# Optimization experiments

Measured on AMD Instinct MI355X. Metric: run time of the kernel, lower is better.

The kernel has to match this reference:

```python
import jax, jax.numpy as jnp
import numpy as np

L, H = 3, 8
B, N, D, E = 4, 256, 128, 128
NH, EH1, EH2 = 512, 512, 512


def _ln(x, g, b):
    m = x.mean(-1, keepdims=True)
    v = ((x - m) ** 2).mean(-1, keepdims=True)
    return (x - m) * jax.lax.rsqrt(v + 1e-5) * g + b


def setup_inputs() -> dict:
    key = jax.random.key(0)
    ks = jax.random.split(key, 16)
    w = lambda k, *s: jax.random.normal(k, s, jnp.float32) * 0.02
    inp = {
        'node_features': jax.random.normal(ks[0], (B, N, D), jnp.float32),
        'edge_features': jax.random.normal(ks[1], (B, N, N, E), jnp.float32),
        'Wqkv_n': w(ks[2], L, D, 3 * D), 'bqkv_n': jnp.zeros((L, 3 * D)),
        'Wqkv_e': w(ks[3], L, E, 3 * D), 'bqkv_e': jnp.zeros((L, 3 * D)),
        'Wo': w(ks[4], L, D, D), 'bo': jnp.zeros((L, D)),
        'Wn1': w(ks[5], L, D, NH), 'bn1': jnp.zeros((L, NH)),
        'Wn2': w(ks[6], L, NH, D), 'bn2': jnp.zeros((L, D)),
        'ln1n_g': jnp.ones((L, D)), 'ln1n_b': jnp.zeros((L, D)),
        'ln2n_g': jnp.ones((L, D)), 'ln2n_b': jnp.zeros((L, D)),
        'We1a': w(ks[7], L, 2 * D + 2 * E, EH1), 'be1a': jnp.zeros((L, EH1)),
        'We1b': w(ks[8], L, EH1, E), 'be1b': jnp.zeros((L, E)),
        'We2a': w(ks[9], L, E, EH2), 'be2a': jnp.zeros((L, EH2)),
        'We2b': w(ks[10], L, EH2, E), 'be2b': jnp.zeros((L, E)),
        'ln1e_g': jnp.ones((L, E)), 'ln1e_b': jnp.zeros((L, E)),
        'ln2e_g': jnp.ones((L, E)), 'ln2e_b': jnp.zeros((L, E)),
    }
    return inp


def reference(node_features, edge_features, Wqkv_n, bqkv_n, Wqkv_e, bqkv_e, Wo, bo,
              Wn1, bn1, Wn2, bn2, ln1n_g, ln1n_b, ln2n_g, ln2n_b,
              We1a, be1a, We1b, be1b, We2a, be2a, We2b, be2b,
              ln1e_g, ln1e_b, ln2e_g, ln2e_b):
    n, e = node_features, edge_features
    b_, N_, D_ = n.shape
    hd = D_ // H
    scale = 1.0 / np.sqrt(hd).astype(np.float32)
    for l in range(Wqkv_n.shape[0]):
        # ---- edge-biased attention ----
        qkv_n = (n @ Wqkv_n[l] + bqkv_n[l]).reshape(b_, N_, H, 3 * hd).transpose(0, 2, 1, 3)  # B,H,N,3hd
        q_n, k_n, v_n = jnp.split(qkv_n, 3, axis=-1)
        qkv_e = (e @ Wqkv_e[l] + bqkv_e[l]).reshape(b_, N_, N_, H, 3 * hd).transpose(0, 3, 1, 2, 4)  # B,H,N,N,3hd
        q_e, k_e, v_e = jnp.split(qkv_e, 3, axis=-1)
        q = q_n[:, :, :, None, :] + q_e  # B,H,N,N,hd
        # NOTE: the original torch code overwrites k with q (`k = q.reshape(...)`),
        # so scores are the squared norm of q; k_n/k_e are dead code. Faithful.
        scores = jnp.einsum('bhijd,bhijd->bhij', q, q) * scale
        att = jax.nn.softmax(scores, axis=-1)
        v = v_n[:, :, None, :, :] + v_e  # B,H,N,N,hd
        out = jnp.einsum('bhij,bhijd->bhid', att, v)  # B,H,N,hd
        out = out.transpose(0, 2, 1, 3).reshape(b_, N_, D_) @ Wo[l] + bo[l]
        n = _ln(n + out, ln1n_g[l], ln1n_b[l])
        ff = jax.nn.relu(n @ Wn1[l] + bn1[l]) @ Wn2[l] + bn2[l]
        n = _ln(n + ff, ln2n_g[l], ln2n_b[l])
        # ---- edge update ----
        src = jnp.broadcast_to(n[:, None, :, :], (b_, N_, N_, D_))  # node j
        tgt = jnp.broadcast_to(n[:, :, None, :], (b_, N_, N_, D_))  # node i
        cat = jnp.concatenate([e, e.transpose(0, 2, 1, 3), src, tgt], axis=-1)
        e1 = jax.nn.relu(cat @ We1a[l] + be1a[l]) @ We1b[l] + be1b[l]
        e = _ln(e + e1, ln1e_g[l], ln1e_b[l])
        e2 = jax.nn.relu(e @ We2a[l] + be2a[l]) @ We2b[l] + be2b[l]
        e = _ln(e + e2, ln2e_g[l], ln2e_b[l])
    return n
```

## Files before the change

kernel.cpp:

```cpp
#include <hip/hip_runtime.h>

typedef unsigned short u16;
typedef __bf16 bf16x8 __attribute__((ext_vector_type(8)));
typedef float f32x4 __attribute__((ext_vector_type(4)));

#define NB 4
#define NN 256
#define DD 128
#define RNN 262144

__device__ __forceinline__ u16 f2b(float f) {
    unsigned u = __builtin_bit_cast(unsigned, f);
    unsigned rb = ((u >> 16) & 1u) + 0x7FFFu;
    return (u16)((u + rb) >> 16);
}
__device__ __forceinline__ float b2f(u16 u) {
    return __builtin_bit_cast(float, ((unsigned)u) << 16);
}
__device__ __forceinline__ u16 b16(float f) {
    __bf16 h = (__bf16)f;
    return __builtin_bit_cast(u16, h);
}
__device__ __forceinline__ unsigned pk2(float a, float b) {
    ushort2 r;
    r.x = b16(a); r.y = b16(b);
    return __builtin_bit_cast(unsigned, r);
}

__device__ __forceinline__ void glds16(const void* g, void* l) {
    __builtin_amdgcn_global_load_lds((const __attribute__((address_space(1))) void*)g,
                                     (__attribute__((address_space(3))) void*)l, 16, 0, 0);
}

__global__ void prep_weights(const float* __restrict__ Wqkv_e, const float* __restrict__ bqkv_e,
                             const float* __restrict__ We1a, const float* __restrict__ We1b,
                             const float* __restrict__ We2a, const float* __restrict__ We2b,
                             u16* wqT, u16* wv, float* bqp, float* bvp,
                             u16* w1f_e1, u16* w2f_e1, u16* w1f_e2, u16* w2f_e2) {
    int l = blockIdx.z, sec = blockIdx.y;
    int idx = blockIdx.x * 256 + threadIdx.x;
    if (sec == 0) {
        if (idx < 16384) {
            int n = idx >> 7, k = idx & 127;
            int col = (n >> 4) * 48 + (n & 15);
            wqT[l * 16384 + n * 128 + k] = f2b(Wqkv_e[l * 49152 + k * 384 + col]);
        }
    } else if (sec == 1) {
        if (idx < 16384) {
            int k = idx >> 7, c = idx & 127;
            int col = (c >> 4) * 48 + 32 + (c & 15);
            wv[l * 16384 + k * 128 + c] = f2b(Wqkv_e[l * 49152 + k * 384 + col]);
        }
        if (idx < 128) {
            bqp[l * 128 + idx] = bqkv_e[l * 384 + (idx >> 4) * 48 + (idx & 15)];
            bvp[l * 128 + idx] = bqkv_e[l * 384 + (idx >> 4) * 48 + 32 + (idx & 15)];
        }
    } else if (sec == 2) {
        if (idx < 131072) {
            int step = idx >> 13, q = step >> 2, kt = step & 3;
            int rem = idx & 8191;
            int nb = rem >> 10, ks = (rem >> 9) & 1, ln = (rem >> 3) & 63, j = rem & 7;
            int n = q * 128 + nb * 16 + (ln & 15);
            int k = kt * 64 + ks * 32 + (ln >> 4) * 8 + j;
            w1f_e1[l * 131072 + idx] = f2b(We1a[l * 262144 + k * 512 + n]);
        }
    } else if (sec == 3) {
        if (idx < 65536) {
            int step = idx >> 13, q = step >> 1, kt2 = step & 1;
            int rem = idx & 8191;
            int cb = rem >> 10, ks = (rem >> 9) & 1, ln = (rem >> 3) & 63, j = rem & 7;
            int c = cb * 16 + (ln & 15);
            int k = q * 128 + kt2 * 64 + ks * 32 + (ln >> 4) * 8 + j;
            w2f_e1[l * 65536 + idx] = f2b(We1b[l * 65536 + k * 128 + c]);
        }
    } else if (sec == 4) {
        if (idx < 65536) {
            int step = idx >> 13, q = step >> 1, kt = step & 1;
            int rem = idx & 8191;
            int nb = rem >> 10, ks = (rem >> 9) & 1, ln = (rem >> 3) & 63, j = rem & 7;
            int n = q * 128 + nb * 16 + (ln & 15);
            int k = kt * 64 + ks * 32 + (ln >> 4) * 8 + j;
            w1f_e2[l * 65536 + idx] = f2b(We2a[l * 65536 + k * 512 + n]);
        }
    } else {
        if (idx < 65536) {
            int step = idx >> 13, q = step >> 1, kt2 = step & 1;
            int rem = idx & 8191;
            int cb = rem >> 10, ks = (rem >> 9) & 1, ln = (rem >> 3) & 63, j = rem & 7;
            int c = cb * 16 + (ln & 15);
            int k = q * 128 + kt2 * 64 + ks * 32 + (ln >> 4) * 8 + j;
            w2f_e2[l * 65536 + idx] = f2b(We2b[l * 65536 + k * 128 + c]);
        }
    }
}

__global__ void init_e(const float4* __restrict__ src, ushort4* __restrict__ dst) {
    const long n4 = 8388608;
    for (long i = (long)blockIdx.x * blockDim.x + threadIdx.x; i < n4; i += (long)gridDim.x * blockDim.x) {
        float4 v = src[i];
        ushort4 o;
        o.x = f2b(v.x); o.y = f2b(v.y); o.z = f2b(v.z); o.w = f2b(v.w);
        dst[i] = o;
    }
}

__global__ void init_n(const float* __restrict__ node, float* __restrict__ nf) {
    int i = blockIdx.x * 256 + threadIdx.x;
    if (i < 131072) nf[i] = node[i];
}

__launch_bounds__(512)
__global__ void pre_node_kernel(const float* __restrict__ nf, const float* __restrict__ We1a,
                                float* __restrict__ preS, float* __restrict__ preT) {
    __shared__ float nr[128];
    int tid = threadIdx.x;
    int row = blockIdx.x;
    if (tid < 128) nr[tid] = nf[(long)row * 128 + tid];
    __syncthreads();
    int c = tid;
    float s = 0.f, t = 0.f;
    const float* Ws = We1a + (long)256 * 512 + c;
    const float* Wt = We1a + (long)384 * 512 + c;
    #pragma unroll 8
    for (int k = 0; k < 128; ++k) {
        float nv = nr[k];
        s += nv * Ws[k * 512];
        t += nv * Wt[k * 512];
    }
    preS[(long)row * 512 + c] = s;
    preT[(long)row * 512 + c] = t;
}

__global__ void qkvn_kernel(const float* __restrict__ nf, const float* __restrict__ W,
                            const float* __restrict__ bias, float* __restrict__ qn, float* __restrict__ vn) {
    __shared__ float nr[128];
    int tid = threadIdx.x;
    int row = blockIdx.x;
    if (tid < 128) nr[tid] = nf[(long)row * 128 + tid];
    __syncthreads();
    int c = tid & 127;
    bool isq = tid < 128;
    int col = (c >> 4) * 48 + (c & 15) + (isq ? 0 : 32);
    float a = bias[col];
    #pragma unroll 8
    for (int k = 0; k < 128; ++k) a += nr[k] * W[k * 384 + col];
    if (isq) qn[(long)row * 128 + c] = a;
    else     vn[(long)row * 128 + c] = a;
}

__launch_bounds__(256, 2)
__global__ void scores_kernel(const u16* __restrict__ ein, const u16* __restrict__ WqT,
                              const float* __restrict__ bqp, const float* __restrict__ qn,
                              float* __restrict__ scoresp) {
    __shared__ u16 As[128 * 64];
    __shared__ u16 Bs[128 * 64];
    int tid = threadIdx.x;
    int wid = tid >> 6, lane = tid & 63;
    int bid = blockIdx.x;
    int jhalf = bid & 1, bi = bid >> 1;
    int b = bi >> 8, i = bi & 255;
    int wr = wid >> 1, wc = wid & 1;

    f32x4 acc[4][4];
    f32x4 z = {0.f, 0.f, 0.f, 0.f};
    #pragma unroll
    for (int m = 0; m < 4; ++m)
        #pragma unroll
        for (int n = 0; n < 4; ++n) acc[m][n] = z;

    const long arow0 = ((long)(b * NN + i) * NN + jhalf * 128);
    for (int kt = 0; kt < 2; ++kt) {
        int k0 = kt << 6;
        #pragma unroll
        for (int p = 0; p < 4; ++p) {
            int r = p * 32 + (tid >> 3);
            int ch = tid & 7;
            const u16* src = ein + (arow0 + r) * 128 + k0 + ((ch ^ (r & 7)) << 3);
            glds16(src, (char*)As + (p << 12) + (wid << 10));
            int n = p * 32 + (tid >> 3);
            const u16* bsrc = WqT + (long)n * 128 + k0 + ((ch ^ (n & 7)) << 3);
            glds16(bsrc, (char*)Bs + (p << 12) + (wid << 10));
        }
        __syncthreads();
        #pragma unroll
        for (int ks = 0; ks < 2; ++ks) {
            bf16x8 af[4], bfr[4];
            #pragma unroll
            for (int m = 0; m < 4; ++m) {
                int r = wr * 64 + m * 16 + (lane & 15);
                int ch = (ks * 4 + (lane >> 4)) ^ (r & 7);
                af[m] = *reinterpret_cast<const bf16x8*>(&As[r * 64 + ch * 8]);
            }
            #pragma unroll
            for (int n = 0; n < 4; ++n) {
                int c = wc * 64 + n * 16 + (lane & 15);
                int ch = (ks * 4 + (lane >> 4)) ^ (c & 7);
                bfr[n] = *reinterpret_cast<const bf16x8*>(&Bs[c * 64 + ch * 8]);
            }
            #pragma unroll
            for (int m = 0; m < 4; ++m)
                #pragma unroll
                for (int n = 0; n < 4; ++n)
                    acc[m][n] = __builtin_amdgcn_mfma_f32_16x16x32_bf16(af[m], bfr[n], acc[m][n], 0, 0, 0);
        }
        __syncthreads();
    }
    const float* qnb = qn + (long)(b * NN + i) * 128;
    #pragma unroll
    for (int m = 0; m < 4; ++m) {
        #pragma unroll
        for (int n = 0; n < 4; ++n) {
            int col = wc * 64 + n * 16 + (lane & 15);
            float add = bqp[col] + qnb[col];
            float sv[4];
            #pragma unroll
            for (int t = 0; t < 4; ++t) { float qv = acc[m][n][t] + add; sv[t] = qv * qv; }
            #pragma unroll
            for (int mk = 1; mk <= 8; mk <<= 1)
                #pragma unroll
                for (int t = 0; t < 4; ++t) sv[t] += __shfl_xor(sv[t], mk);
            if ((lane & 15) == 0) {
                int head = wc * 4 + n;
                int jb = jhalf * 128 + wr * 64 + m * 16 + ((lane >> 4) << 2);
                long sbase = ((long)(b * 8 + head) * 256 + i) * 256 + jb;
                #pragma unroll
                for (int t = 0; t < 4; ++t) scoresp[sbase + t] = sv[t] * 0.25f;
            }
        }
    }
}

__launch_bounds__(256)
__global__ void attn_pv_kernel(const float* __restrict__ scoresp, const u16* __restrict__ ein,
                               const float* __restrict__ vn, const u16* __restrict__ Wv,
                               const float* __restrict__ bvp, float* __restrict__ attn_o) {
    __shared__ float s_s[8 * 256];
    __shared__ float g_s[8 * 128];
    __shared__ float part[256];
    int tid = threadIdx.x;
    int b = blockIdx.x >> 8, i = blockIdx.x & 255;
    for (int v = tid; v < 2048; v += 256) {
        int h = v >> 8, j = v & 255;
        s_s[v] = scoresp[((long)(b * 8 + h) * 256 + i) * 256 + j];
    }
    __syncthreads();
    {
        int h = tid >> 5, lg = tid & 31;
        float vals[8], mx = -1e30f;
        #pragma unroll
        for (int t = 0; t < 8; ++t) { vals[t] = s_s[h * 256 + lg + t * 32]; mx = fmaxf(mx, vals[t]); }
        #pragma unroll
        for (int mk = 16; mk; mk >>= 1) mx = fmaxf(mx, __shfl_xor(mx, mk));
        float sum = 0.f;
        #pragma unroll
        for (int t = 0; t < 8; ++t) { vals[t] = __expf(vals[t] - mx); sum += vals[t]; }
        #pragma unroll
        for (int mk = 16; mk; mk >>= 1) sum += __shfl_xor(sum, mk);
        float inv = 1.f / sum;
        #pragma unroll
        for (int t = 0; t < 8; ++t) s_s[h * 256 + lg + t * 32] = vals[t] * inv;
    }
    __syncthreads();
    {
        int k = tid & 127, h0 = tid >> 7;
        const u16* erow = ein + ((long)(b * NN + i) * NN) * 128 + k;
        float a0 = 0, a1 = 0, a2 = 0, a3 = 0;
        for (int j = 0; j < 256; ++j) {
            float ev = b2f(erow[(long)j * 128]);
            a0 += s_s[(h0    ) * 256 + j] * ev;
            a1 += s_s[(h0 + 2) * 256 + j] * ev;
            a2 += s_s[(h0 + 4) * 256 + j] * ev;
            a3 += s_s[(h0 + 6) * 256 + j] * ev;
        }
        g_s[(h0    ) * 128 + k] = a0;
        g_s[(h0 + 2) * 128 + k] = a1;
        g_s[(h0 + 4) * 128 + k] = a2;
        g_s[(h0 + 6) * 128 + k] = a3;
    }
    __syncthreads();
    {
        int c = tid & 127, half = tid >> 7;
        int h = c >> 4;
        float a = 0.f;
        for (int j = half * 128; j < half * 128 + 128; ++j)
            a += s_s[h * 256 + j] * vn[((long)(b * NN + j)) * 128 + c];
        for (int k = half * 64; k < half * 64 + 64; ++k)
            a += g_s[h * 128 + k] * b2f(Wv[k * 128 + c]);
        part[tid] = a;
    }
    __syncthreads();
    if (tid < 128)
        attn_o[((long)(b * NN + i)) * 128 + tid] = part[tid] + part[128 + tid] + bvp[tid];
}

__launch_bounds__(256)
__global__ void node_kernel(const float* __restrict__ attn_o, float* __restrict__ nf,
                            const float* __restrict__ Wo, const float* __restrict__ bo,
                            const float* __restrict__ Wn1, const float* __restrict__ bn1,
                            const float* __restrict__ Wn2, const float* __restrict__ bn2,
                            const float* __restrict__ g1, const float* __restrict__ b1,
                            const float* __restrict__ g2, const float* __restrict__ b2) {
    __shared__ float ao[128], nr[128], n1[128], hb[512];
    __shared__ float red[8];
    int tid = threadIdx.x;
    int wid = tid >> 6, lane = tid & 63;
    long base = (long)blockIdx.x * 128;
    if (tid < 128) { ao[tid] = attn_o[base + tid]; nr[tid] = nf[base + tid]; }
    __syncthreads();
    float x = 0.f;
    if (tid < 128) {
        float a = bo[tid];
        #pragma unroll 8
        for (int k = 0; k < 128; ++k) a += ao[k] * Wo[k * 128 + tid];
        x = nr[tid] + a;
    }
    float s = (tid < 128) ? x : 0.f, q = (tid < 128) ? x * x : 0.f;
    #pragma unroll
    for (int mk = 1; mk <= 32; mk <<= 1) { s += __shfl_xor(s, mk); q += __shfl_xor(q, mk); }
    if (lane == 0) { red[wid * 2] = s; red[wid * 2 + 1] = q; }
    __syncthreads();
    float sum = red[0] + red[2] + red[4] + red[6];
    float sq  = red[1] + red[3] + red[5] + red[7];
    float mean = sum * (1.f / 128.f);
    float var = sq * (1.f / 128.f) - mean * mean;
    float rs = rsqrtf(var + 1e-5f);
    __syncthreads();
    if (tid < 128) n1[tid] = (x - mean) * rs * g1[tid] + b1[tid];
    __syncthreads();
    for (int c = tid; c < 512; c += 256) {
        float a = bn1[c];
        #pragma unroll 8
        for (int k = 0; k < 128; ++k) a += n1[k] * Wn1[k * 512 + c];
        hb[c] = a > 0.f ? a : 0.f;
    }
    __syncthreads();
    float y = 0.f;
    if (tid < 128) {
        float a = bn2[tid];
        #pragma unroll 8
        for (int k = 0; k < 512; ++k) a += hb[k] * Wn2[k * 128 + tid];
        y = n1[tid] + a;
    }
    float s2 = (tid < 128) ? y : 0.f, q2 = (tid < 128) ? y * y : 0.f;
    #pragma unroll
    for (int mk = 1; mk <= 32; mk <<= 1) { s2 += __shfl_xor(s2, mk); q2 += __shfl_xor(q2, mk); }
    if (lane == 0) { red[wid * 2] = s2; red[wid * 2 + 1] = q2; }
    __syncthreads();
    sum = red[0] + red[2] + red[4] + red[6];
    sq  = red[1] + red[3] + red[5] + red[7];
    mean = sum * (1.f / 128.f);
    var = sq * (1.f / 128.f) - mean * mean;
    rs = rsqrtf(var + 1e-5f);
    if (tid < 128) {
        float o = (y - mean) * rs * g2[tid] + b2[tid];
        nf[base + tid] = o;
    }
}

__launch_bounds__(256, 3)
__global__ void fused_mlp6(const u16* __restrict__ W1aF, const float* __restrict__ b1a,
                           const u16* __restrict__ W1bF, const float* __restrict__ b1b,
                           const u16* __restrict__ W2aF, const float* __restrict__ b2a,
                           const u16* __restrict__ W2bF, const float* __restrict__ b2b,
                           const u16* __restrict__ ein,
                           const float* __restrict__ preS, const float* __restrict__ preT,
                           const float* __restrict__ ln1g, const float* __restrict__ ln1b,
                           const float* __restrict__ ln2g, const float* __restrict__ ln2b,
                           u16* __restrict__ e_dst) {
    __shared__ __align__(16) u16 A_lds[16384];
    __shared__ __align__(16) u16 Hs[8192];
    __shared__ float psum[256], psq[256];

    int tid = threadIdx.x;
    int wid = tid >> 6, lane = tid & 63;
    long row0 = (long)blockIdx.x * 64;
    int b = (int)(row0 >> 16);
    int rem0 = (int)(row0 & 65535);
    int i_ = rem0 >> 8, j0 = rem0 & 255;

    #pragma unroll
    for (int kt = 0; kt < 4; ++kt)
        #pragma unroll
        for (int pp = 0; pp < 2; ++pp) {
            int r = pp * 32 + (tid >> 3);
            int ch = tid & 7;
            long ridx = (kt < 2) ? (long)(b * NN + i_) * NN + (j0 + r)
                                 : (long)(b * NN + (j0 + r)) * NN + i_;
            const u16* src = ein + ridx * DD + ((kt & 1) << 6) + ((ch ^ (r & 7)) << 3);
            glds16(src, (char*)A_lds + kt * 8192 + (pp << 12) + (wid << 10));
        }
    asm volatile("s_waitcnt vmcnt(0)" ::: "memory");
    __builtin_amdgcn_sched_barrier(0);
    __builtin_amdgcn_s_barrier();
    __builtin_amdgcn_sched_barrier(0);

    const u16* w1a = W1aF + (wid * 2) * 1024 + lane * 8;
    const u16* w1b = W1bF + (wid * 2) * 1024 + lane * 8;
    const u16* w2a = W2aF + (wid * 2) * 1024 + lane * 8;
    const u16* w2b = W2bF + (wid * 2) * 1024 + lane * 8;

    f32x4 z = {0.f, 0.f, 0.f, 0.f};
    f32x4 acc1[2][4], acc2[4][2];
    bf16x8 afA[4], afB[4], g2A[4], g2B[4];

    auto FR4 = [&](bf16x8 (&d)[4], const u16* base, int step) {
        const u16* p = base + (step << 13);
        d[0] = *reinterpret_cast<const bf16x8*>(p);
        d[1] = *reinterpret_cast<const bf16x8*>(p + 1024);
        d[2] = *reinterpret_cast<const bf16x8*>(p + 512);
        d[3] = *reinterpret_cast<const bf16x8*>(p + 1536);
    };
    auto G1K = [&](bf16x8 (&cur)[4], int reg) {
        #pragma unroll
        for (int ks = 0; ks < 2; ++ks) {
            bf16x8 bfr[4];
            #pragma unroll
            for (int rf = 0; rf < 4; ++rf) {
                int r = rf * 16 + (lane & 15);
                int ch = (ks * 4 + (lane >> 4)) ^ (r & 7);
                bfr[rf] = *reinterpret_cast<const bf16x8*>(&A_lds[reg * 4096 + r * 64 + ch * 8]);
            }
            #pragma unroll
            for (int mn = 0; mn < 2; ++mn)
                #pragma unroll
                for (int rf = 0; rf < 4; ++rf)
                    acc1[mn][rf] = __builtin_amdgcn_mfma_f32_16x16x32_bf16(cur[ks * 2 + mn], bfr[rf], acc1[mn][rf], 0, 0, 0);
        }
    };
    auto G2K = [&](bf16x8 (&w)[4], int kt2) {
        #pragma unroll
        for (int ks = 0; ks < 2; ++ks) {
            bf16x8 af2[4];
            #pragma unroll
            for (int rf = 0; rf < 4; ++rf) {
                int r = rf * 16 + (lane & 15);
                int c8 = kt2 * 8 + ks * 4 + (lane >> 4);
                int cs = (c8 & 8) | ((c8 ^ r) & 7);
                af2[rf] = *reinterpret_cast<const bf16x8*>((const char*)Hs + r * 256 + cs * 16);
            }
            #pragma unroll
            for (int rf = 0; rf < 4; ++rf)
                #pragma unroll
                for (int cf = 0; cf < 2; ++cf)
                    acc2[rf][cf] = __builtin_amdgcn_mfma_f32_16x16x32_bf16(af2[rf], w[ks * 2 + cf], acc2[rf][cf], 0, 0, 0);
        }
    };
    auto EPI = [&](int q, const float* bias, bool wp) {
        #pragma unroll
        for (int mn = 0; mn < 2; ++mn) {
            int nl0 = wid * 32 + mn * 16 + ((lane >> 4) << 2);
            int n0g = (q << 7) + nl0;
            float4 bb = *reinterpret_cast<const float4*>(&bias[n0g]);
            if (wp) {
                float4 pt = *reinterpret_cast<const float4*>(&preT[(long)(b * NN + i_) * 512 + n0g]);
                bb.x += pt.x; bb.y += pt.y; bb.z += pt.z; bb.w += pt.w;
            }
            #pragma unroll
            for (int rf = 0; rf < 4; ++rf) {
                int r = rf * 16 + (lane & 15);
                float b0 = bb.x, b1_ = bb.y, b2_ = bb.z, b3 = bb.w;
                if (wp) {
                    float4 ps = *reinterpret_cast<const float4*>(&preS[(long)(b * NN + j0 + r) * 512 + n0g]);
                    b0 += ps.x; b1_ += ps.y; b2_ += ps.z; b3 += ps.w;
                }
                float v0 = acc1[mn][rf][0] + b0; v0 = v0 > 0.f ? v0 : 0.f;
                float v1 = acc1[mn][rf][1] + b1_; v1 = v1 > 0.f ? v1 : 0.f;
                float v2 = acc1[mn][rf][2] + b2_; v2 = v2 > 0.f ? v2 : 0.f;
                float v3 = acc1[mn][rf][3] + b3; v3 = v3 > 0.f ? v3 : 0.f;
                uint2 pk;
                pk.x = pk2(v0, v1);
                pk.y = pk2(v2, v3);
                int c8 = nl0 >> 3;
                int cs = (c8 & 8) | ((c8 ^ r) & 7);
                *reinterpret_cast<uint2*>((char*)Hs + r * 256 + cs * 16 + (nl0 & 7) * 2) = pk;
            }
        }
    };
    auto LNA = [&](const float* bias, int rb) {
        #pragma unroll
        for (int rf = 0; rf < 4; ++rf) {
            float sv[4] = {0.f, 0.f, 0.f, 0.f}, qv[4] = {0.f, 0.f, 0.f, 0.f};
            #pragma unroll
            for (int cf = 0; cf < 2; ++cf) {
                int c = wid * 32 + cf * 16 + (lane & 15);
                float bb = bias[c];
                int kk = c & 63, kreg = rb + (c >> 6);
                #pragma unroll
                for (int t = 0; t < 4; ++t) {
                    int r = rf * 16 + ((lane >> 4) << 2) + t;
                    float er = b2f(A_lds[kreg * 4096 + r * 64 + (((kk >> 3) ^ (r & 7)) << 3) + (kk & 7)]);
                    float x = acc2[rf][cf][t] + bb + er;
                    acc2[rf][cf][t] = x;
                    sv[t] += x;
                    qv[t] += x * x;
                }
            }
            #pragma unroll
            for (int mk = 1; mk <= 8; mk <<= 1)
                #pragma unroll
                for (int t = 0; t < 4; ++t) { sv[t] += __shfl_xor(sv[t], mk); qv[t] += __shfl_xor(qv[t], mk); }
            if ((lane & 15) == 0) {
                #pragma unroll
                for (int t = 0; t < 4; ++t) {
                    int r = rf * 16 + ((lane >> 4) << 2) + t;
                    psum[r * 4 + wid] = sv[t];
                    psq[r * 4 + wid] = qv[t];
                }
            }
        }
    };

    #pragma unroll
    for (int rf = 0; rf < 4; ++rf) { acc2[rf][0] = z; acc2[rf][1] = z; }
    FR4(afA, w1a, 0);
    for (int q = 0; q < 4; ++q) {
        #pragma unroll
        for (int mn = 0; mn < 2; ++mn)
            #pragma unroll
            for (int rf = 0; rf < 4; ++rf) acc1[mn][rf] = z;
        FR4(afB, w1a, q * 4 + 1); G1K(afA, 0);
        FR4(afA, w1a, q * 4 + 2); G1K(afB, 1);
        FR4(afB, w1a, q * 4 + 3); G1K(afA, 2);
        G1K(afB, 3);
        FR4(g2A, w1b, q * 2 + 0);
        if (q) {
            __builtin_amdgcn_sched_barrier(0);
            __builtin_amdgcn_s_barrier();
            __builtin_amdgcn_sched_barrier(0);
        }
        EPI(q, b1a, true);
        asm volatile("s_waitcnt lgkmcnt(0)" ::: "memory");
        __builtin_amdgcn_sched_barrier(0);
        __builtin_amdgcn_s_barrier();
        __builtin_amdgcn_sched_barrier(0);
        FR4(g2B, w1b, q * 2 + 1);
        G2K(g2A, 0);
        if (q < 3) FR4(afA, w1a, (q + 1) * 4);
        G2K(g2B, 1);
    }

    LNA(b1b, 0);
    __syncthreads();
    #pragma unroll
    for (int rf = 0; rf < 4; ++rf) {
        #pragma unroll
        for (int t = 0; t < 4; ++t) {
            int r = rf * 16 + ((lane >> 4) << 2) + t;
            float sum = psum[r * 4] + psum[r * 4 + 1] + psum[r * 4 + 2] + psum[r * 4 + 3];
            float sq  = psq[r * 4] + psq[r * 4 + 1] + psq[r * 4 + 2] + psq[r * 4 + 3];
            float mean = sum * (1.f / 128.f);
            float var = sq * (1.f / 128.f) - mean * mean;
            float rs = rsqrtf(var + 1e-5f);
            #pragma unroll
            for (int cf = 0; cf < 2; ++cf) {
                int c = wid * 32 + cf * 16 + (lane & 15);
                float o = (acc2[rf][cf][t] - mean) * rs * ln1g[c] + ln1b[c];
                int kk = c & 63;
                A_lds[(2 + (c >> 6)) * 4096 + r * 64 + (((kk >> 3) ^ (r & 7)) << 3) + (kk & 7)] = b16(o);
            }
        }
    }
    __syncthreads();

    #pragma unroll
    for (int rf = 0; rf < 4; ++rf) { acc2[rf][0] = z; acc2[rf][1] = z; }
    FR4(afA, w2a, 0);
    for (int q = 0; q < 4; ++q) {
        #pragma unroll
        for (int mn = 0; mn < 2; ++mn)
            #pragma unroll
            for (int rf = 0; rf < 4; ++rf) acc1[mn][rf] = z;
        FR4(afB, w2a, q * 2 + 1); G1K(afA, 2);
        G1K(afB, 3);
        FR4(g2A, w2b, q * 2 + 0);
        if (q) {
            __builtin_amdgcn_sched_barrier(0);
            __builtin_amdgcn_s_barrier();
            __builtin_amdgcn_sched_barrier(0);
        }
        EPI(q, b2a, false);
        asm volatile("s_waitcnt lgkmcnt(0)" ::: "memory");
        __builtin_amdgcn_sched_barrier(0);
        __builtin_amdgcn_s_barrier();
        __builtin_amdgcn_sched_barrier(0);
        FR4(g2B, w2b, q * 2 + 1);
        G2K(g2A, 0);
        if (q < 3) FR4(afA, w2a, (q + 1) * 2);
        G2K(g2B, 1);
    }

    LNA(b2b, 2);
    __syncthreads();
    #pragma unroll
    for (int rf = 0; rf < 4; ++rf) {
        #pragma unroll
        for (int t = 0; t < 4; ++t) {
            int r = rf * 16 + ((lane >> 4) << 2) + t;
            float sum = psum[r * 4] + psum[r * 4 + 1] + psum[r * 4 + 2] + psum[r * 4 + 3];
            float sq  = psq[r * 4] + psq[r * 4 + 1] + psq[r * 4 + 2] + psq[r * 4 + 3];
            float mean = sum * (1.f / 128.f);
            float var = sq * (1.f / 128.f) - mean * mean;
            float rs = rsqrtf(var + 1e-5f);
            #pragma unroll
            for (int cf = 0; cf < 2; ++cf) {
                int c = wid * 32 + cf * 16 + (lane & 15);
                float o = (acc2[rf][cf][t] - mean) * rs * ln2g[c] + ln2b[c];
                A_lds[r * 128 + c] = b16(o);
            }
        }
    }
    __syncthreads();
    #pragma unroll
    for (int pp = 0; pp < 4; ++pp) {
        ulonglong2 v = *reinterpret_cast<const ulonglong2*>((char*)A_lds + (pp << 12) + tid * 16);
        *reinterpret_cast<ulonglong2*>((char*)e_dst + row0 * 256 + (pp << 12) + tid * 16) = v;
    }
}

extern "C" void kernel_launch(void* const* d_in, const int* in_sizes, int n_in,
                              void* d_out, int out_size, void* d_ws, size_t ws_size,
                              hipStream_t stream) {
    (void)in_sizes; (void)n_in; (void)out_size; (void)ws_size;
    const float* node   = (const float*)d_in[0];
    const float* edge   = (const float*)d_in[1];
    const float* Wqkv_n = (const float*)d_in[2];
    const float* bqkv_n = (const float*)d_in[3];
    const float* Wqkv_e = (const float*)d_in[4];
    const float* bqkv_e = (const float*)d_in[5];
    const float* Wo     = (const float*)d_in[6];
    const float* bo     = (const float*)d_in[7];
    const float* Wn1    = (const float*)d_in[8];
    const float* bn1    = (const float*)d_in[9];
    const float* Wn2    = (const float*)d_in[10];
    const float* bn2    = (const float*)d_in[11];
    const float* ln1n_g = (const float*)d_in[12];
    const float* ln1n_b = (const float*)d_in[13];
    const float* ln2n_g = (const float*)d_in[14];
    const float* ln2n_b = (const float*)d_in[15];
    const float* We1a   = (const float*)d_in[16];
    const float* be1a   = (const float*)d_in[17];
    const float* We1b   = (const float*)d_in[18];
    const float* be1b   = (const float*)d_in[19];
    const float* We2a   = (const float*)d_in[20];
    const float* be2a   = (const float*)d_in[21];
    const float* We2b   = (const float*)d_in[22];
    const float* be2b   = (const float*)d_in[23];
    const float* ln1e_g = (const float*)d_in[24];
    const float* ln1e_b = (const float*)d_in[25];
    const float* ln2e_g = (const float*)d_in[26];
    const float* ln2e_b = (const float*)d_in[27];

    size_t off = 0;
    char* wsb = (char*)d_ws;
    auto alloc = [&](size_t bytes) -> void* {
        void* p = wsb + off;
        off = (off + bytes + 255) & ~(size_t)255;
        return p;
    };
    u16* eb0      = (u16*)alloc((size_t)RNN * 128 * 2);
    u16* eb1      = (u16*)alloc((size_t)RNN * 128 * 2);
    float* scoresp= (float*)alloc((size_t)2097152 * 4);
    float* qn     = (float*)alloc(131072 * 4);
    float* vn     = (float*)alloc(131072 * 4);
    float* attn_o = (float*)alloc(131072 * 4);
    float* nf     = (float*)alloc(131072 * 4);
    float* preS   = (float*)alloc((size_t)1024 * 512 * 4);
    float* preT   = (float*)alloc((size_t)1024 * 512 * 4);
    u16* wqT      = (u16*)alloc(3 * 16384 * 2);
    u16* wv       = (u16*)alloc(3 * 16384 * 2);
    float* bqp    = (float*)alloc(3 * 128 * 4);
    float* bvp    = (float*)alloc(3 * 128 * 4);
    u16* w1f_e1   = (u16*)alloc(3 * 131072ull * 2);
    u16* w2f_e1   = (u16*)alloc(3 * 65536 * 2);
    u16* w1f_e2   = (u16*)alloc(3 * 65536 * 2);
    u16* w2f_e2   = (u16*)alloc(3 * 65536 * 2);

    {
        dim3 g(512, 6, 3);
        prep_weights<<<g, 256, 0, stream>>>(Wqkv_e, bqkv_e, We1a, We1b, We2a, We2b,
                                            wqT, wv, bqp, bvp, w1f_e1, w2f_e1, w1f_e2, w2f_e2);
    }
    init_e<<<2048, 256, 0, stream>>>((const float4*)edge, (ushort4*)eb0);
    init_n<<<512, 256, 0, stream>>>(node, nf);

    for (int l = 0; l < 3; ++l) {
        u16* ein  = (l & 1) ? eb1 : eb0;
        u16* eout = (l & 1) ? eb0 : eb1;
        qkvn_kernel<<<1024, 256, 0, stream>>>(nf, Wqkv_n + l * 49152, bqkv_n + l * 384, qn, vn);
        scores_kernel<<<2048, 256, 0, stream>>>(ein, wqT + l * 16384, bqp + l * 128, qn, scoresp);
        attn_pv_kernel<<<1024, 256, 0, stream>>>(scoresp, ein, vn, wv + l * 16384, bvp + l * 128, attn_o);
        node_kernel<<<1024, 256, 0, stream>>>(attn_o, nf,
                                              Wo + l * 16384, bo + l * 128,
                                              Wn1 + l * 65536, bn1 + l * 512,
                                              Wn2 + l * 65536, bn2 + l * 128,
                                              ln1n_g + l * 128, ln1n_b + l * 128,
                                              ln2n_g + l * 128, ln2n_b + l * 128);
        pre_node_kernel<<<1024, 512, 0, stream>>>(nf, We1a + (size_t)l * 262144, preS, preT);
        fused_mlp6<<<4096, 256, 0, stream>>>(w1f_e1 + l * 131072, be1a + l * 512,
                                             w2f_e1 + l * 65536, be1b + l * 128,
                                             w1f_e2 + l * 65536, be2a + l * 512,
                                             w2f_e2 + l * 65536, be2b + l * 128,
                                             ein, preS, preT,
                                             ln1e_g + l * 128, ln1e_b + l * 128,
                                             ln2e_g + l * 128, ln2e_b + l * 128,
                                             eout);
    }
    hipMemcpyAsync(d_out, nf, 131072 * sizeof(float), hipMemcpyDeviceToDevice, stream);
}
```

Before: 1.304 ms.

## Halve fused edge-MLP row tile and split node matvecs across all threads

The fused edge MLP kernel now processes 32 rows per block instead of 64. It doubles the grid, halves the LDS buffers and accumulators, and raises the launch-bounds occupancy hint from 3 to 4 blocks. Each block still streams all weight fragments, so weight traffic per row doubles in exchange for more resident blocks and less register and LDS pressure. Separately, the Wo and Wn2 matvecs in node_kernel are split into two K-halves so all 256 threads work instead of 128, with partial sums reduced through shared memory.

```diff
diff --git a/kernel.cpp b/kernel.cpp
--- a/kernel.cpp
+++ b/kernel.cpp
@@ -301,19 +301,23 @@
                             const float* __restrict__ g1, const float* __restrict__ b1,
                             const float* __restrict__ g2, const float* __restrict__ b2) {
     __shared__ float ao[128], nr[128], n1[128], hb[512];
+    __shared__ float part[256];
     __shared__ float red[8];
     int tid = threadIdx.x;
     int wid = tid >> 6, lane = tid & 63;
     long base = (long)blockIdx.x * 128;
     if (tid < 128) { ao[tid] = attn_o[base + tid]; nr[tid] = nf[base + tid]; }
     __syncthreads();
+    {
+        int c = tid & 127, half = tid >> 7;
+        float a = 0.f;
+        #pragma unroll 8
+        for (int k = half * 64; k < half * 64 + 64; ++k) a += ao[k] * Wo[k * 128 + c];
+        part[tid] = a;
+    }
+    __syncthreads();
     float x = 0.f;
-    if (tid < 128) {
-        float a = bo[tid];
-        #pragma unroll 8
-        for (int k = 0; k < 128; ++k) a += ao[k] * Wo[k * 128 + tid];
-        x = nr[tid] + a;
-    }
+    if (tid < 128) x = nr[tid] + bo[tid] + part[tid] + part[128 + tid];
     float s = (tid < 128) ? x : 0.f, q = (tid < 128) ? x * x : 0.f;
     #pragma unroll
     for (int mk = 1; mk <= 32; mk <<= 1) { s += __shfl_xor(s, mk); q += __shfl_xor(q, mk); }
@@ -334,13 +338,16 @@
         hb[c] = a > 0.f ? a : 0.f;
     }
     __syncthreads();
+    {
+        int c = tid & 127, half = tid >> 7;
+        float a = 0.f;
+        #pragma unroll 8
+        for (int k = half * 256; k < half * 256 + 256; ++k) a += hb[k] * Wn2[k * 128 + c];
+        part[tid] = a;
+    }
+    __syncthreads();
     float y = 0.f;
-    if (tid < 128) {
-        float a = bn2[tid];
-        #pragma unroll 8
-        for (int k = 0; k < 512; ++k) a += hb[k] * Wn2[k * 128 + tid];
-        y = n1[tid] + a;
-    }
+    if (tid < 128) y = n1[tid] + bn2[tid] + part[tid] + part[128 + tid];
     float s2 = (tid < 128) ? y : 0.f, q2 = (tid < 128) ? y * y : 0.f;
     #pragma unroll
     for (int mk = 1; mk <= 32; mk <<= 1) { s2 += __shfl_xor(s2, mk); q2 += __shfl_xor(q2, mk); }
@@ -357,7 +364,7 @@
     }
 }
 
-__launch_bounds__(256, 3)
+__launch_bounds__(256, 4)
 __global__ void fused_mlp6(const u16* __restrict__ W1aF, const float* __restrict__ b1a,
                            const u16* __restrict__ W1bF, const float* __restrict__ b1b,
                            const u16* __restrict__ W2aF, const float* __restrict__ b2a,
@@ -367,28 +374,26 @@
                            const float* __restrict__ ln1g, const float* __restrict__ ln1b,
                            const float* __restrict__ ln2g, const float* __restrict__ ln2b,
                            u16* __restrict__ e_dst) {
-    __shared__ __align__(16) u16 A_lds[16384];
-    __shared__ __align__(16) u16 Hs[8192];
-    __shared__ float psum[256], psq[256];
+    __shared__ __align__(16) u16 A_lds[8192];
+    __shared__ __align__(16) u16 Hs[4096];
+    __shared__ float psum[128], psq[128];
 
     int tid = threadIdx.x;
     int wid = tid >> 6, lane = tid & 63;
-    long row0 = (long)blockIdx.x * 64;
+    long row0 = (long)blockIdx.x * 32;
     int b = (int)(row0 >> 16);
     int rem0 = (int)(row0 & 65535);
     int i_ = rem0 >> 8, j0 = rem0 & 255;
 
     #pragma unroll
-    for (int kt = 0; kt < 4; ++kt)
-        #pragma unroll
-        for (int pp = 0; pp < 2; ++pp) {
-            int r = pp * 32 + (tid >> 3);
-            int ch = tid & 7;
-            long ridx = (kt < 2) ? (long)(b * NN + i_) * NN + (j0 + r)
-                                 : (long)(b * NN + (j0 + r)) * NN + i_;
-            const u16* src = ein + ridx * DD + ((kt & 1) << 6) + ((ch ^ (r & 7)) << 3);
-            glds16(src, (char*)A_lds + kt * 8192 + (pp << 12) + (wid << 10));
-        }
+    for (int kt = 0; kt < 4; ++kt) {
+        int r = tid >> 3;
+        int ch = tid & 7;
+        long ridx = (kt < 2) ? (long)(b * NN + i_) * NN + (j0 + r)
+                             : (long)(b * NN + (j0 + r)) * NN + i_;
+        const u16* src = ein + ridx * DD + ((kt & 1) << 6) + ((ch ^ (r & 7)) << 3);
+        glds16(src, (char*)A_lds + kt * 4096 + (wid << 10));
+    }
     asm volatile("s_waitcnt vmcnt(0)" ::: "memory");
     __builtin_amdgcn_sched_barrier(0);
     __builtin_amdgcn_s_barrier();
@@ -400,7 +405,7 @@
     const u16* w2b = W2bF + (wid * 2) * 1024 + lane * 8;
 
     f32x4 z = {0.f, 0.f, 0.f, 0.f};
-    f32x4 acc1[2][4], acc2[4][2];
+    f32x4 acc1[2][2], acc2[2][2];
     bf16x8 afA[4], afB[4], g2A[4], g2B[4];
 
     auto FR4 = [&](bf16x8 (&d)[4], const u16* base, int step) {
@@ -413,33 +418,33 @@
     auto G1K = [&](bf16x8 (&cur)[4], int reg) {
         #pragma unroll
         for (int ks = 0; ks < 2; ++ks) {
-            bf16x8 bfr[4];
-            #pragma unroll
-            for (int rf = 0; rf < 4; ++rf) {
+            bf16x8 bfr[2];
+            #pragma unroll
+            for (int rf = 0; rf < 2; ++rf) {
                 int r = rf * 16 + (lane & 15);
                 int ch = (ks * 4 + (lane >> 4)) ^ (r & 7);
-                bfr[rf] = *reinterpret_cast<const bf16x8*>(&A_lds[reg * 4096 + r * 64 + ch * 8]);
+                bfr[rf] = *reinterpret_cast<const bf16x8*>(&A_lds[reg * 2048 + r * 64 + ch * 8]);
             }
             #pragma unroll
             for (int mn = 0; mn < 2; ++mn)
                 #pragma unroll
-                for (int rf = 0; rf < 4; ++rf)
+                for (int rf = 0; rf < 2; ++rf)
                     acc1[mn][rf] = __builtin_amdgcn_mfma_f32_16x16x32_bf16(cur[ks * 2 + mn], bfr[rf], acc1[mn][rf], 0, 0, 0);
         }
     };
     auto G2K = [&](bf16x8 (&w)[4], int kt2) {
         #pragma unroll
         for (int ks = 0; ks < 2; ++ks) {
-            bf16x8 af2[4];
-            #pragma unroll
-            for (int rf = 0; rf < 4; ++rf) {
+            bf16x8 af2[2];
+            #pragma unroll
+            for (int rf = 0; rf < 2; ++rf) {
                 int r = rf * 16 + (lane & 15);
                 int c8 = kt2 * 8 + ks * 4 + (lane >> 4);
                 int cs = (c8 & 8) | ((c8 ^ r) & 7);
                 af2[rf] = *reinterpret_cast<const bf16x8*>((const char*)Hs + r * 256 + cs * 16);
             }
             #pragma unroll
-            for (int rf = 0; rf < 4; ++rf)
+            for (int rf = 0; rf < 2; ++rf)
                 #pragma unroll
                 for (int cf = 0; cf < 2; ++cf)
                     acc2[rf][cf] = __builtin_amdgcn_mfma_f32_16x16x32_bf16(af2[rf], w[ks * 2 + cf], acc2[rf][cf], 0, 0, 0);
@@ -456,7 +461,7 @@
                 bb.x += pt.x; bb.y += pt.y; bb.z += pt.z; bb.w += pt.w;
             }
             #pragma unroll
-            for (int rf = 0; rf < 4; ++rf) {
+            for (int rf = 0; rf < 2; ++rf) {
                 int r = rf * 16 + (lane & 15);
                 float b0 = bb.x, b1_ = bb.y, b2_ = bb.z, b3 = bb.w;
                 if (wp) {
@@ -478,7 +483,7 @@
     };
     auto LNA = [&](const float* bias, int rb) {
         #pragma unroll
-        for (int rf = 0; rf < 4; ++rf) {
+        for (int rf = 0; rf < 2; ++rf) {
             float sv[4] = {0.f, 0.f, 0.f, 0.f}, qv[4] = {0.f, 0.f, 0.f, 0.f};
             #pragma unroll
             for (int cf = 0; cf < 2; ++cf) {
@@ -488,7 +493,7 @@
                 #pragma unroll
                 for (int t = 0; t < 4; ++t) {
                     int r = rf * 16 + ((lane >> 4) << 2) + t;
-                    float er = b2f(A_lds[kreg * 4096 + r * 64 + (((kk >> 3) ^ (r & 7)) << 3) + (kk & 7)]);
+                    float er = b2f(A_lds[kreg * 2048 + r * 64 + (((kk >> 3) ^ (r & 7)) << 3) + (kk & 7)]);
                     float x = acc2[rf][cf][t] + bb + er;
                     acc2[rf][cf][t] = x;
                     sv[t] += x;
@@ -511,13 +516,13 @@
     };
 
     #pragma unroll
-    for (int rf = 0; rf < 4; ++rf) { acc2[rf][0] = z; acc2[rf][1] = z; }
+    for (int rf = 0; rf < 2; ++rf) { acc2[rf][0] = z; acc2[rf][1] = z; }
     FR4(afA, w1a, 0);
     for (int q = 0; q < 4; ++q) {
         #pragma unroll
         for (int mn = 0; mn < 2; ++mn)
             #pragma unroll
-            for (int rf = 0; rf < 4; ++rf) acc1[mn][rf] = z;
+            for (int rf = 0; rf < 2; ++rf) acc1[mn][rf] = z;
         FR4(afB, w1a, q * 4 + 1); G1K(afA, 0);
         FR4(afA, w1a, q * 4 + 2); G1K(afB, 1);
         FR4(afB, w1a, q * 4 + 3); G1K(afA, 2);
@@ -542,7 +547,7 @@
     LNA(b1b, 0);
     __syncthreads();
     #pragma unroll
-    for (int rf = 0; rf < 4; ++rf) {
+    for (int rf = 0; rf < 2; ++rf) {
         #pragma unroll
         for (int t = 0; t < 4; ++t) {
             int r = rf * 16 + ((lane >> 4) << 2) + t;
@@ -556,20 +561,20 @@
                 int c = wid * 32 + cf * 16 + (lane & 15);
                 float o = (acc2[rf][cf][t] - mean) * rs * ln1g[c] + ln1b[c];
                 int kk = c & 63;
-                A_lds[(2 + (c >> 6)) * 4096 + r * 64 + (((kk >> 3) ^ (r & 7)) << 3) + (kk & 7)] = b16(o);
-            }
-        }
-    }
-    __syncthreads();
-
-    #pragma unroll
-    for (int rf = 0; rf < 4; ++rf) { acc2[rf][0] = z; acc2[rf][1] = z; }
+                A_lds[(2 + (c >> 6)) * 2048 + r * 64 + (((kk >> 3) ^ (r & 7)) << 3) + (kk & 7)] = b16(o);
+            }
+        }
+    }
+    __syncthreads();
+
+    #pragma unroll
+    for (int rf = 0; rf < 2; ++rf) { acc2[rf][0] = z; acc2[rf][1] = z; }
     FR4(afA, w2a, 0);
     for (int q = 0; q < 4; ++q) {
         #pragma unroll
         for (int mn = 0; mn < 2; ++mn)
             #pragma unroll
-            for (int rf = 0; rf < 4; ++rf) acc1[mn][rf] = z;
+            for (int rf = 0; rf < 2; ++rf) acc1[mn][rf] = z;
         FR4(afB, w2a, q * 2 + 1); G1K(afA, 2);
         G1K(afB, 3);
         FR4(g2A, w2b, q * 2 + 0);
@@ -592,7 +597,7 @@
     LNA(b2b, 2);
     __syncthreads();
     #pragma unroll
-    for (int rf = 0; rf < 4; ++rf) {
+    for (int rf = 0; rf < 2; ++rf) {
         #pragma unroll
         for (int t = 0; t < 4; ++t) {
             int r = rf * 16 + ((lane >> 4) << 2) + t;
@@ -611,7 +616,7 @@
     }
     __syncthreads();
     #pragma unroll
-    for (int pp = 0; pp < 4; ++pp) {
+    for (int pp = 0; pp < 2; ++pp) {
         ulonglong2 v = *reinterpret_cast<const ulonglong2*>((char*)A_lds + (pp << 12) + tid * 16);
         *reinterpret_cast<ulonglong2*>((char*)e_dst + row0 * 256 + (pp << 12) + tid * 16) = v;
     }
@@ -696,7 +701,7 @@
                                               ln1n_g + l * 128, ln1n_b + l * 128,
                                               ln2n_g + l * 128, ln2n_b + l * 128);
         pre_node_kernel<<<1024, 512, 0, stream>>>(nf, We1a + (size_t)l * 262144, preS, preT);
-        fused_mlp6<<<4096, 256, 0, stream>>>(w1f_e1 + l * 131072, be1a + l * 512,
+        fused_mlp6<<<8192, 256, 0, stream>>>(w1f_e1 + l * 131072, be1a + l * 512,
                                              w2f_e1 + l * 65536, be1b + l * 128,
                                              w1f_e2 + l * 65536, be2a + l * 512,
                                              w2f_e2 + l * 65536, be2b + l * 128,
```

Measured after the change: 1.327 ms. No clear change (+1.8%).
